# Optimization experiments

Hardware: AMD Instinct MI355X
Metric: run time of the kernel (lower is better)

The kernel has to match this reference:

```python
import jax, jax.numpy as jnp
import numpy as np

NUM_HEADS = 16
D_MODEL = 1024
HEAD_DIM = D_MODEL // NUM_HEADS
EMB = 1024
B, L = 2, 2048


def setup_inputs() -> dict:
    key = jax.random.key(0)
    k1, k2, k3 = jax.random.split(key, 3)
    scale_in = 1.0 / np.sqrt(EMB)
    scale_out = 1.0 / np.sqrt(D_MODEL)
    return {
        "x": jax.random.normal(k1, (B, L, EMB), dtype=jnp.float32),
        "W_qkv": jax.random.normal(k2, (EMB, 3 * D_MODEL), dtype=jnp.float32) * scale_in,
        "b_qkv": jnp.zeros((3 * D_MODEL,), dtype=jnp.float32),
        "W_out": jax.random.normal(k3, (D_MODEL, EMB), dtype=jnp.float32) * scale_out,
        "b_out": jnp.zeros((EMB,), dtype=jnp.float32),
    }


def reference(x, W_qkv, b_qkv, W_out, b_out):
    Bn, Ln, _ = x.shape
    qkv = x @ W_qkv + b_qkv  # [B, L, 3*d_model]
    q = qkv[:, :, :D_MODEL].reshape(Bn, Ln, NUM_HEADS, HEAD_DIM)
    k = qkv[:, :, D_MODEL:2 * D_MODEL].reshape(Bn, Ln, NUM_HEADS, HEAD_DIM)
    v = qkv[:, :, 2 * D_MODEL:].reshape(Bn, Ln, NUM_HEADS, HEAD_DIM)
    scores = jnp.einsum('bqhd,bkhd->bhqk', q, k)  # [B, H, L, L]
    attn = jax.nn.softmax(scores / jnp.sqrt(jnp.float32(HEAD_DIM)), axis=-1)
    out = jnp.einsum('bhqk,bkhd->bqhd', attn, v).reshape(Bn, Ln, D_MODEL)
    return out @ W_out + b_out
```

## Files before the change

kernel.cpp:

```cpp
#include <hip/hip_runtime.h>
#include <stdint.h>

#define B_   2
#define L_   2048
#define H_   16
#define D_   64
#define EMB_ 1024
#define DM_  1024
#define N3_  3072
#define TOK_ 4096

typedef unsigned short u16;
typedef unsigned int u32;
typedef __attribute__((ext_vector_type(4))) float f32x4;
typedef __attribute__((ext_vector_type(8))) short s16x8;
typedef __attribute__((ext_vector_type(4))) u32 u32x4;
typedef __attribute__((ext_vector_type(2))) u32 u32x2;
typedef __attribute__((ext_vector_type(4))) u16 u16x4;

#define MFMA(a,b,c) __builtin_amdgcn_mfma_f32_16x16x32_bf16(a,b,c,0,0,0)

#define AS1 __attribute__((address_space(1)))
#define AS3 __attribute__((address_space(3)))
#define GLLDS(g, l) __builtin_amdgcn_global_load_lds( \
    (const AS1 u32*)(const void*)(g), (AS3 u32*)(void*)(l), 16, 0, 0)

#define QSCALE 0.18033688011f

static __device__ __forceinline__ u16 f2bf(float f) {
  u32 u = __builtin_bit_cast(u32, f);
  u = (u + 0x7fffu + ((u >> 16) & 1u)) >> 16;
  return (u16)u;
}

static __device__ __forceinline__ u32 pack2bf(float a, float b) {
#if __has_builtin(__builtin_amdgcn_cvt_pk_bf16_f32)
  auto v = __builtin_amdgcn_cvt_pk_bf16_f32(a, b);
  return __builtin_bit_cast(u32, v);
#else
  return (u32)f2bf(a) | ((u32)f2bf(b) << 16);
#endif
}

static __device__ __forceinline__ float fexp2(float x) {
#if __has_builtin(__builtin_amdgcn_exp2f)
  return __builtin_amdgcn_exp2f(x);
#else
  float r;
  asm("v_exp_f32 %0, %1" : "=v"(r) : "v"(x));
  return r;
#endif
}

__global__ __launch_bounds__(256) void k_prep(
    const float* __restrict__ x,   u16* __restrict__ xb,
    const float* __restrict__ Wq,  u16* __restrict__ wqT,
    const float* __restrict__ Wo,  u16* __restrict__ woT)
{
  const int blk = blockIdx.x, tid = threadIdx.x;
  if (blk < 4096) {
    int i = (blk * 256 + tid) * 4;
    float4 v = *(const float4*)(x + i);
    ushort4 o;
    o.x = f2bf(v.x); o.y = f2bf(v.y); o.z = f2bf(v.z); o.w = f2bf(v.w);
    *(ushort4*)(xb + i) = o;
    return;
  }
  __shared__ float tile[32][33];
  const float* in;
  u16* out;
  int R, C, bx, by;
  if (blk < 4096 + 3072) {
    int t = blk - 4096;
    in = Wq; out = wqT; R = EMB_; C = N3_;
    bx = t % 96; by = t / 96;
  } else {
    int t = blk - 7168;
    in = Wo; out = woT; R = DM_; C = DM_;
    bx = t & 31; by = t >> 5;
  }
  int c0 = bx * 32, r0 = by * 32;
  int tx = tid & 31, ty = tid >> 5;
  #pragma unroll
  for (int i = 0; i < 32; i += 8)
    tile[ty + i][tx] = in[(size_t)(r0 + ty + i) * C + (c0 + tx)];
  __syncthreads();
  #pragma unroll
  for (int i = 0; i < 32; i += 8)
    out[(size_t)(c0 + ty + i) * R + (r0 + tx)] = f2bf(tile[tx][ty + i]);
}

template<int EPI>
__global__ __launch_bounds__(256, 2) void k_gemm(
    const u16* __restrict__ A, const u16* __restrict__ Bt,
    const float* __restrict__ bias, int M, int N, int K,
    float* __restrict__ Cf,
    u16* __restrict__ Qo, u16* __restrict__ Ko, u16* __restrict__ Vo)
{
  const int tid = threadIdx.x;
  const int wave = tid >> 6, lane = tid & 63;
  const int lr = lane & 15, lk = lane >> 4;
  const int wr = wave >> 1, wc = wave & 1;
  const int m0 = blockIdx.y * 128, n0 = blockIdx.x * 128;

  __shared__ u16 As[128 * 32];
  __shared__ u16 Bs[128 * 32];

  f32x4 acc[4][4] = {};

  const int srow = wave * 32 + (lane >> 2);
  const int schunk = (lane & 3) * 8;
  const u16* gA0 = A  + (size_t)(m0 + srow) * K + schunk;
  const u16* gB0 = Bt + (size_t)(n0 + srow) * K + schunk;
  const u16* gA1 = gA0 + (size_t)16 * K;
  const u16* gB1 = gB0 + (size_t)16 * K;
  u16* lA = As + wave * (32 * 32);
  u16* lB = Bs + wave * (32 * 32);

  for (int k0 = 0; k0 < K; k0 += 32) {
    __syncthreads();
    GLLDS(gA0 + k0, lA);
    GLLDS(gA1 + k0, lA + 16 * 32);
    GLLDS(gB0 + k0, lB);
    GLLDS(gB1 + k0, lB + 16 * 32);
    __syncthreads();

    s16x8 af[4], bf[4];
    #pragma unroll
    for (int mi = 0; mi < 4; ++mi)
      af[mi] = *(const s16x8*)(As + (wr * 64 + mi * 16 + lr) * 32 + lk * 8);
    #pragma unroll
    for (int ni = 0; ni < 4; ++ni)
      bf[ni] = *(const s16x8*)(Bs + (wc * 64 + ni * 16 + lr) * 32 + lk * 8);
    #pragma unroll
    for (int mi = 0; mi < 4; ++mi)
      #pragma unroll
      for (int ni = 0; ni < 4; ++ni)
        acc[mi][ni] = MFMA(af[mi], bf[ni], acc[mi][ni]);
  }

  const int mbase = m0 + wr * 64 + lk * 4;
  #pragma unroll
  for (int ni = 0; ni < 4; ++ni) {
    int gn = n0 + wc * 64 + ni * 16 + lr;
    float bz = bias[gn];
    #pragma unroll
    for (int mi = 0; mi < 4; ++mi) {
      #pragma unroll
      for (int r = 0; r < 4; ++r) {
        int gm = mbase + mi * 16 + r;
        float v = acc[mi][ni][r] + bz;
        if (EPI == 1) {
          Cf[(size_t)gm * N + gn] = v;
        } else {
          int sec = gn >> 10, cm = gn & 1023;
          int h = cm >> 6, d = cm & 63;
          int b = gm >> 11, l = gm & 2047;
          int bh = b * H_ + h;
          if (sec == 0)      Qo[((size_t)bh * L_ + l) * D_ + d] = f2bf(v * QSCALE);
          else if (sec == 1) Ko[((size_t)bh * L_ + l) * D_ + d] = f2bf(v);
          else               Vo[((size_t)bh * D_ + d) * L_ + l] = f2bf(v);
        }
      }
    }
  }
}

__global__ __launch_bounds__(256, 4) void k_flash(
    const u16* __restrict__ Q, const u16* __restrict__ Kb,
    const u16* __restrict__ Vt, u16* __restrict__ AO)
{
  const int tid = threadIdx.x;
  const int wave = tid >> 6, lane = tid & 63;
  const int lr = lane & 15, lk = lane >> 4;
  const int blk = blockIdx.x;
  const int idx = blk >> 3;
  const int bh = (blk & 7) * 4 + (idx >> 5);
  const int qt = idx & 31;
  const int b = bh >> 4, h = bh & 15;
  const u16* Qh = Q  + (size_t)bh * L_ * D_;
  const u16* Kh = Kb + (size_t)bh * L_ * D_;
  const u16* Vh = Vt + (size_t)bh * D_ * L_;

  __shared__ u16 Ks[2][64 * 64];
  __shared__ u16 Vs[2][64 * 64];
  __shared__ u16 Ps[64 * 64];

  const int qrow0 = qt * 64 + wave * 16;
  s16x8 qf[2];
  #pragma unroll
  for (int ks = 0; ks < 2; ++ks)
    qf[ks] = *(const s16x8*)(Qh + (size_t)(qrow0 + lr) * D_ + ks * 32 + lk * 8);

  f32x4 acco[4] = {};
  float lst = 0.f;

  const int srow0 = wave * 16 + (lane >> 3);
  const int gch8 = (((lane & 7) ^ ((lane >> 3) & 7)) * 8);
  u16* kd0 = (u16*)Ks[0] + wave * (16 * 64);
  u16* kd1 = (u16*)Ks[1] + wave * (16 * 64);
  u16* vd0 = (u16*)Vs[0] + wave * (16 * 64);
  u16* vd1 = (u16*)Vs[1] + wave * (16 * 64);

  const int ck0 = (lk ^ (lr & 7)) * 8;
  const int sxor = (lr & 7) << 1;
  u16* PsW = Ps + wave * (16 * 64);

  GLLDS(Kh + (size_t)srow0 * 64 + gch8,        kd0);
  GLLDS(Kh + (size_t)(srow0 + 8) * 64 + gch8,  kd0 + 8 * 64);
  GLLDS(Vh + (size_t)srow0 * L_ + gch8,        vd0);
  GLLDS(Vh + (size_t)(srow0 + 8) * L_ + gch8,  vd0 + 8 * 64);

  int buf = 0;
  for (int t0 = 0; t0 < L_; t0 += 64, buf ^= 1) {
    __syncthreads();

    if (t0 + 64 < L_) {
      const int tn = t0 + 64;
      u16* kd = buf ? kd0 : kd1;
      u16* vd = buf ? vd0 : vd1;
      GLLDS(Kh + (size_t)(tn + srow0) * 64 + gch8,       kd);
      GLLDS(Kh + (size_t)(tn + srow0 + 8) * 64 + gch8,   kd + 8 * 64);
      GLLDS(Vh + ((size_t)srow0 * L_ + tn + gch8),       vd);
      GLLDS(Vh + ((size_t)(srow0 + 8) * L_ + tn + gch8), vd + 8 * 64);
    }

    const u16* Kbuf = (const u16*)Ks[buf];
    f32x4 accs[4] = {};
    s16x8 kf[4][2];
    #pragma unroll
    for (int mi = 0; mi < 4; ++mi) {
      const u16* rp = Kbuf + (mi * 16 + lr) * 64;
      kf[mi][0] = *(const s16x8*)(rp + ck0);
      kf[mi][1] = *(const s16x8*)(rp + (ck0 ^ 32));
    }
    #pragma unroll
    for (int mi = 0; mi < 4; ++mi) {
      accs[mi] = MFMA(kf[mi][0], qf[0], accs[mi]);
      accs[mi] = MFMA(kf[mi][1], qf[1], accs[mi]);
    }

    #pragma unroll
    for (int mi = 0; mi < 4; ++mi) {
      float p0 = fexp2(accs[mi][0]);
      float p1 = fexp2(accs[mi][1]);
      float p2 = fexp2(accs[mi][2]);
      float p3 = fexp2(accs[mi][3]);
      lst += (p0 + p1) + (p2 + p3);
      u32x2 pk = { pack2bf(p0, p1), pack2bf(p2, p3) };
      *(u32x2*)(PsW + lr * 64 + (((4 * mi + lk) ^ sxor) * 4)) = pk;
    }

    const u16* Vbuf = (const u16*)Vs[buf];
    s16x8 vf[4][2], pf[2];
    #pragma unroll
    for (int di = 0; di < 4; ++di) {
      const u16* rp = Vbuf + (di * 16 + lr) * 64;
      vf[di][0] = *(const s16x8*)(rp + ck0);
      vf[di][1] = *(const s16x8*)(rp + (ck0 ^ 32));
    }
    pf[0] = *(const s16x8*)(PsW + lr * 64 + (((2 * lk) ^ sxor) * 4));
    pf[1] = *(const s16x8*)(PsW + lr * 64 + (((8 + 2 * lk) ^ sxor) * 4));
    #pragma unroll
    for (int di = 0; di < 4; ++di) {
      acco[di] = MFMA(vf[di][0], pf[0], acco[di]);
      acco[di] = MFMA(vf[di][1], pf[1], acco[di]);
    }
  }

  lst += __shfl_xor(lst, 16);
  lst += __shfl_xor(lst, 32);
  float rl = 1.0f / lst;
  const int q = qrow0 + lr;
  #pragma unroll
  for (int di = 0; di < 4; ++di) {
    u16x4 o;
    #pragma unroll
    for (int r = 0; r < 4; ++r)
      o[r] = f2bf(acco[di][r] * rl);
    *(u16x4*)(AO + (size_t)(b * L_ + q) * DM_ + h * D_ + di * 16 + lk * 4) = o;
  }
}

extern "C" void kernel_launch(void* const* d_in, const int* in_sizes, int n_in,
                              void* d_out, int out_size, void* d_ws, size_t ws_size,
                              hipStream_t stream)
{
  const float* x    = (const float*)d_in[0];
  const float* Wqkv = (const float*)d_in[1];
  const float* bqkv = (const float*)d_in[2];
  const float* Wout = (const float*)d_in[3];
  const float* bout = (const float*)d_in[4];
  float* out = (float*)d_out;

  u16* xb  = (u16*)d_ws;
  u16* wqT = xb  + (size_t)TOK_ * EMB_;
  u16* woT = wqT + (size_t)N3_ * EMB_;
  u16* qb  = woT + (size_t)DM_ * EMB_;
  u16* kb  = qb  + (size_t)B_ * H_ * L_ * D_;
  u16* vt  = kb  + (size_t)B_ * H_ * L_ * D_;
  u16* ao  = vt  + (size_t)B_ * H_ * L_ * D_;

  k_prep<<<4096 + 3072 + 1024, 256, 0, stream>>>(x, xb, Wqkv, wqT, Wout, woT);
  k_gemm<0><<<dim3(N3_ / 128, TOK_ / 128), 256, 0, stream>>>(
      xb, wqT, bqkv, TOK_, N3_, EMB_, nullptr, qb, kb, vt);
  k_flash<<<1024, 256, 0, stream>>>(qb, kb, vt, ao);
  k_gemm<1><<<dim3(DM_ / 128, TOK_ / 128), 256, 0, stream>>>(
      ao, woT, bout, TOK_, DM_, EMB_, out, nullptr, nullptr, nullptr);
}
```

Measured before the change: 205.9 us.

## Process 128 query rows per flash block to reuse K/V tiles across two groups

```diff
diff --git a/kernel.cpp b/kernel.cpp
--- a/kernel.cpp
+++ b/kernel.cpp
@@ -166,7 +166,7 @@
   }
 }
 
-__global__ __launch_bounds__(256, 4) void k_flash(
+__global__ __launch_bounds__(256, 2) void k_flash(
     const u16* __restrict__ Q, const u16* __restrict__ Kb,
     const u16* __restrict__ Vt, u16* __restrict__ AO)
 {
@@ -175,8 +175,8 @@
   const int lr = lane & 15, lk = lane >> 4;
   const int blk = blockIdx.x;
   const int idx = blk >> 3;
-  const int bh = (blk & 7) * 4 + (idx >> 5);
-  const int qt = idx & 31;
+  const int bh = (blk & 7) * 4 + (idx >> 4);
+  const int qt = idx & 15;
   const int b = bh >> 4, h = bh & 15;
   const u16* Qh = Q  + (size_t)bh * L_ * D_;
   const u16* Kh = Kb + (size_t)bh * L_ * D_;
@@ -184,16 +184,18 @@
 
   __shared__ u16 Ks[2][64 * 64];
   __shared__ u16 Vs[2][64 * 64];
-  __shared__ u16 Ps[64 * 64];
-
-  const int qrow0 = qt * 64 + wave * 16;
-  s16x8 qf[2];
-  #pragma unroll
-  for (int ks = 0; ks < 2; ++ks)
-    qf[ks] = *(const s16x8*)(Qh + (size_t)(qrow0 + lr) * D_ + ks * 32 + lk * 8);
-
-  f32x4 acco[4] = {};
-  float lst = 0.f;
+  __shared__ u16 Ps[128 * 64];
+
+  const int qrow0 = qt * 128 + wave * 32;
+  s16x8 qf[2][2];
+  #pragma unroll
+  for (int g = 0; g < 2; ++g)
+    #pragma unroll
+    for (int ks = 0; ks < 2; ++ks)
+      qf[g][ks] = *(const s16x8*)(Qh + (size_t)(qrow0 + g * 16 + lr) * D_ + ks * 32 + lk * 8);
+
+  f32x4 acco[2][4] = {};
+  float lst[2] = {0.f, 0.f};
 
   const int srow0 = wave * 16 + (lane >> 3);
   const int gch8 = (((lane & 7) ^ ((lane >> 3) & 7)) * 8);
@@ -204,7 +206,7 @@
 
   const int ck0 = (lk ^ (lr & 7)) * 8;
   const int sxor = (lr & 7) << 1;
-  u16* PsW = Ps + wave * (16 * 64);
+  u16* PsW = Ps + wave * (32 * 64);
 
   GLLDS(Kh + (size_t)srow0 * 64 + gch8,        kd0);
   GLLDS(Kh + (size_t)(srow0 + 8) * 64 + gch8,  kd0 + 8 * 64);
@@ -226,7 +228,7 @@
     }
 
     const u16* Kbuf = (const u16*)Ks[buf];
-    f32x4 accs[4] = {};
+    f32x4 accs[2][4] = {};
     s16x8 kf[4][2];
     #pragma unroll
     for (int mi = 0; mi < 4; ++mi) {
@@ -235,50 +237,66 @@
       kf[mi][1] = *(const s16x8*)(rp + (ck0 ^ 32));
     }
     #pragma unroll
-    for (int mi = 0; mi < 4; ++mi) {
-      accs[mi] = MFMA(kf[mi][0], qf[0], accs[mi]);
-      accs[mi] = MFMA(kf[mi][1], qf[1], accs[mi]);
-    }
-
-    #pragma unroll
-    for (int mi = 0; mi < 4; ++mi) {
-      float p0 = fexp2(accs[mi][0]);
-      float p1 = fexp2(accs[mi][1]);
-      float p2 = fexp2(accs[mi][2]);
-      float p3 = fexp2(accs[mi][3]);
-      lst += (p0 + p1) + (p2 + p3);
-      u32x2 pk = { pack2bf(p0, p1), pack2bf(p2, p3) };
-      *(u32x2*)(PsW + lr * 64 + (((4 * mi + lk) ^ sxor) * 4)) = pk;
+    for (int mi = 0; mi < 4; ++mi)
+      #pragma unroll
+      for (int g = 0; g < 2; ++g) {
+        accs[g][mi] = MFMA(kf[mi][0], qf[g][0], accs[g][mi]);
+        accs[g][mi] = MFMA(kf[mi][1], qf[g][1], accs[g][mi]);
+      }
+
+    #pragma unroll
+    for (int g = 0; g < 2; ++g) {
+      const int prow = (g * 16 + lr) * 64;
+      #pragma unroll
+      for (int mi = 0; mi < 4; ++mi) {
+        float p0 = fexp2(accs[g][mi][0]);
+        float p1 = fexp2(accs[g][mi][1]);
+        float p2 = fexp2(accs[g][mi][2]);
+        float p3 = fexp2(accs[g][mi][3]);
+        lst[g] += (p0 + p1) + (p2 + p3);
+        u32x2 pk = { pack2bf(p0, p1), pack2bf(p2, p3) };
+        *(u32x2*)(PsW + prow + (((4 * mi + lk) ^ sxor) * 4)) = pk;
+      }
     }
 
     const u16* Vbuf = (const u16*)Vs[buf];
-    s16x8 vf[4][2], pf[2];
+    s16x8 vf[4][2], pf[2][2];
     #pragma unroll
     for (int di = 0; di < 4; ++di) {
       const u16* rp = Vbuf + (di * 16 + lr) * 64;
       vf[di][0] = *(const s16x8*)(rp + ck0);
       vf[di][1] = *(const s16x8*)(rp + (ck0 ^ 32));
     }
-    pf[0] = *(const s16x8*)(PsW + lr * 64 + (((2 * lk) ^ sxor) * 4));
-    pf[1] = *(const s16x8*)(PsW + lr * 64 + (((8 + 2 * lk) ^ sxor) * 4));
+    #pragma unroll
+    for (int g = 0; g < 2; ++g) {
+      const int prow = (g * 16 + lr) * 64;
+      pf[g][0] = *(const s16x8*)(PsW + prow + (((2 * lk) ^ sxor) * 4));
+      pf[g][1] = *(const s16x8*)(PsW + prow + (((8 + 2 * lk) ^ sxor) * 4));
+    }
+    #pragma unroll
+    for (int di = 0; di < 4; ++di)
+      #pragma unroll
+      for (int g = 0; g < 2; ++g) {
+        acco[g][di] = MFMA(vf[di][0], pf[g][0], acco[g][di]);
+        acco[g][di] = MFMA(vf[di][1], pf[g][1], acco[g][di]);
+      }
+  }
+
+  #pragma unroll
+  for (int g = 0; g < 2; ++g) {
+    float l = lst[g];
+    l += __shfl_xor(l, 16);
+    l += __shfl_xor(l, 32);
+    float rl = 1.0f / l;
+    const int q = qrow0 + g * 16 + lr;
     #pragma unroll
     for (int di = 0; di < 4; ++di) {
-      acco[di] = MFMA(vf[di][0], pf[0], acco[di]);
-      acco[di] = MFMA(vf[di][1], pf[1], acco[di]);
-    }
-  }
-
-  lst += __shfl_xor(lst, 16);
-  lst += __shfl_xor(lst, 32);
-  float rl = 1.0f / lst;
-  const int q = qrow0 + lr;
-  #pragma unroll
-  for (int di = 0; di < 4; ++di) {
-    u16x4 o;
-    #pragma unroll
-    for (int r = 0; r < 4; ++r)
-      o[r] = f2bf(acco[di][r] * rl);
-    *(u16x4*)(AO + (size_t)(b * L_ + q) * DM_ + h * D_ + di * 16 + lk * 4) = o;
+      u16x4 o;
+      #pragma unroll
+      for (int r = 0; r < 4; ++r)
+        o[r] = f2bf(acco[g][di][r] * rl);
+      *(u16x4*)(AO + (size_t)(b * L_ + q) * DM_ + h * D_ + di * 16 + lk * 4) = o;
+    }
   }
 }
 
@@ -304,7 +322,7 @@
   k_prep<<<4096 + 3072 + 1024, 256, 0, stream>>>(x, xb, Wqkv, wqT, Wout, woT);
   k_gemm<0><<<dim3(N3_ / 128, TOK_ / 128), 256, 0, stream>>>(
       xb, wqT, bqkv, TOK_, N3_, EMB_, nullptr, qb, kb, vt);
-  k_flash<<<1024, 256, 0, stream>>>(qb, kb, vt, ao);
+  k_flash<<<512, 256, 0, stream>>>(qb, kb, vt, ao);
   k_gemm<1><<<dim3(DM_ / 128, TOK_ / 128), 256, 0, stream>>>(
       ao, woT, bout, TOK_, DM_, EMB_, out, nullptr, nullptr, nullptr);
 }
```

Measured after the change: 198.7 us. 1.04x faster.
